# Performance work log

Measured on AMD Instinct MI355X. Metric: run time of the kernel, lower is better.

Reference implementation:

```python
import jax, jax.numpy as jnp
import numpy as np

jax.config.update("jax_enable_x64", True)

VOCAB_R_MAX = 3.0
EPS = 1e-8


def _sanitize(x):
    # torch.nan_to_num(x, nan=0.0, posinf=10000.0, neginf=-10000.0)
    return jnp.nan_to_num(x, nan=0.0, posinf=10000.0, neginf=-10000.0)


def setup_inputs() -> dict:
    key = jax.random.key(0)
    k1, k2 = jax.random.split(key, 2)
    B, L, V, n = 2, 512, 50257, 768
    hidden_states = jax.random.normal(k1, (B, L, n + 1), dtype=jnp.float32)
    # nn.Parameter(torch.randn(V, n) * 0.01) -- tangent vectors
    weight = jax.random.normal(k2, (V, n), dtype=jnp.float32) * 0.01
    # init_temp = 1/sqrt(n_embd)
    logit_scale = jnp.asarray(1.0 / np.sqrt(n), dtype=jnp.float32)
    return {"hidden_states": hidden_states, "weight": weight, "logit_scale": logit_scale}


def _exp_map_zero(v_spatial, max_tangent_norm):
    # Lorentz exp map at origin (curvature -1), tangent vector (0, v_spatial).
    # Norm is clamped to max_tangent_norm (geodesic radius ceiling).
    r = jnp.linalg.norm(v_spatial, axis=-1, keepdims=True)  # [V,1]
    rc = jnp.minimum(r, max_tangent_norm)
    dirv = v_spatial / jnp.maximum(r, EPS)
    return jnp.concatenate([jnp.cosh(rc), jnp.sinh(rc) * dirv], axis=-1)  # [V, n+1]


def _ensure_lorentz(x):
    # Project onto the hyperboloid: x0 = sqrt(1 + ||x_spatial||^2)
    sp = x[..., 1:]
    t = jnp.sqrt(1.0 + jnp.sum(sp * sp, axis=-1, keepdims=True))
    return jnp.concatenate([t, sp], axis=-1)


def reference(hidden_states, weight, logit_scale):
    x = _ensure_lorentz(_sanitize(hidden_states))          # [B,L,n+1]
    w = _sanitize(_exp_map_zero(weight, VOCAB_R_MAX))       # [V,n+1]

    x64 = x.astype(jnp.float64)
    w64 = w.astype(jnp.float64)
    # Minkowski inner product split into time/space einsums (as in source)
    time_inner = jnp.einsum('blt,vt->blv', x64[..., :1], w64[:, :1])
    space_inner = jnp.einsum('bls,vs->blv', x64[..., 1:], w64[:, 1:])
    inner = space_inner - time_inner                        # [B,L,V] fp64

    tau = jnp.clip(logit_scale, 0.01, 2.5).astype(jnp.float64)
    logits = (inner * tau).astype(hidden_states.dtype)
    return _sanitize(logits)
```

## Files before the change

kernel.cpp:

```cpp
#include <hip/hip_runtime.h>
#include <hip/hip_bf16.h>
#include <cstdint>
#include <cstddef>
#include <cstring>

typedef __attribute__((ext_vector_type(4))) float f32x4;
typedef __attribute__((ext_vector_type(8))) short bf16x8;

#define KDIM 768
#define BM 128
#define BN 128
#define BK 64

static __device__ __forceinline__ float sani(float x) {
  if (__builtin_isnan(x)) return 0.0f;
  if (__builtin_isinf(x)) return x > 0.0f ? 1.0e4f : -1.0e4f;
  return x;
}

static __device__ __forceinline__ unsigned short f2bf(float x) {
  unsigned u = __builtin_bit_cast(unsigned, x);
  unsigned r = 0x7FFFu + ((u >> 16) & 1u);
  return (unsigned short)((u + r) >> 16);
}


__global__ __launch_bounds__(256) void prep_x_kernel(
    const float* __restrict__ h, unsigned short* __restrict__ xl,
    float* __restrict__ tx) {
  const int row = blockIdx.x;
  const int t = threadIdx.x;
  const int swz = (row & 7) << 3;
  const float* src = h + (size_t)row * (KDIM + 1) + 1;
  float v0 = sani(src[t]);
  float v1 = sani(src[t + 256]);
  float v2 = sani(src[t + 512]);
  float ss = v0 * v0 + v1 * v1 + v2 * v2;
#pragma unroll
  for (int off = 32; off > 0; off >>= 1) ss += __shfl_down(ss, off);
  __shared__ float red[4];
  if ((t & 63) == 0) red[t >> 6] = ss;
  __syncthreads();
  if (t == 0) {
    float total = red[0] + red[1] + red[2] + red[3];
    tx[row] = sqrtf(1.0f + total);
  }
  unsigned short* dst = xl + (size_t)row * KDIM;
  dst[t ^ swz]         = f2bf(v0);
  dst[(t + 256) ^ swz] = f2bf(v1);
  dst[(t + 512) ^ swz] = f2bf(v2);
}

__global__ __launch_bounds__(256) void prep_w_kernel(
    const float* __restrict__ w, unsigned short* __restrict__ wl,
    float* __restrict__ cw, int V) {
  const int row = blockIdx.x;
  const int t = threadIdx.x;
  const int swz = (row & 7) << 3;
  unsigned short* dst = wl + (size_t)row * KDIM;
  if (row >= V) {
    dst[t] = 0; dst[t + 256] = 0; dst[t + 512] = 0;
    if (t == 0) cw[row] = 0.0f;
    return;
  }
  const float* src = w + (size_t)row * KDIM;
  float v0 = src[t];
  float v1 = src[t + 256];
  float v2 = src[t + 512];
  float ss = v0 * v0 + v1 * v1 + v2 * v2;
#pragma unroll
  for (int off = 32; off > 0; off >>= 1) ss += __shfl_down(ss, off);
  __shared__ float red[4];
  if ((t & 63) == 0) red[t >> 6] = ss;
  __syncthreads();
  float total = red[0] + red[1] + red[2] + red[3];
  float r = sqrtf(total);
  float rc = fminf(r, 3.0f);
  float sc = sinhf(rc) / fmaxf(r, 1e-8f);
  dst[t ^ swz]         = f2bf(sani(v0 * sc));
  dst[(t + 256) ^ swz] = f2bf(sani(v1 * sc));
  dst[(t + 512) ^ swz] = f2bf(sani(v2 * sc));
  if (t == 0) cw[row] = sani(coshf(rc));
}

#define GLD16(gp, sp)                                               \
  __builtin_amdgcn_global_load_lds(                                 \
      (const __attribute__((address_space(1))) void*)(gp),          \
      (__attribute__((address_space(3))) void*)(sp), 16, 0, 0)

__global__ __launch_bounds__(256) void gemm_kernel(
    const unsigned short* __restrict__ xl, const unsigned short* __restrict__ wl,
    const float* __restrict__ tx, const float* __restrict__ cw,
    const float* __restrict__ ls, float* __restrict__ out,
    int V, int Mtiles, int nwg8) {
  __shared__ unsigned short As[BM * BK];
  __shared__ unsigned short Bs[BN * BK];

  const int tid = threadIdx.x;
  const int lane = tid & 63;
  const int wid = tid >> 6;
  const int wr = wid >> 1;
  const int wc = wid & 1;

  const int g = blockIdx.x;
  const int L = (g & 7) * nwg8 + (g >> 3);
  const int bm = L & (Mtiles - 1);
  const int bn = L / Mtiles;

  const int l15 = lane & 15;
  const int lq = lane >> 4;
  const int srow = lane >> 3;
  const int scol = (lane & 7) * 8;
  const int swz = (l15 & 7) << 3;

  f32x4 acc[4][4];
#pragma unroll
  for (int i = 0; i < 4; ++i)
#pragma unroll
    for (int j = 0; j < 4; ++j) acc[i][j] = (f32x4){0.f, 0.f, 0.f, 0.f};

  const size_t a_row0 = (size_t)bm * BM;
  const size_t b_row0 = (size_t)bn * BN;

  for (int kt = 0; kt < KDIM / BK; ++kt) {
    const int kbase = kt * BK;
#pragma unroll
    for (int c = 0; c < 4; ++c) {
      const int chunk = wid * 4 + c;
      const int row = chunk * 8 + srow;
      GLD16(xl + (a_row0 + row) * KDIM + kbase + scol, &As[chunk * 512]);
      GLD16(wl + (b_row0 + row) * KDIM + kbase + scol, &Bs[chunk * 512]);
    }
    asm volatile("s_waitcnt vmcnt(0)" ::: "memory");
    __syncthreads();
#pragma unroll
    for (int kk = 0; kk < 2; ++kk) {
      const int koff = (kk * 32 + lq * 8) ^ swz;
      bf16x8 af[4], bfr[4];
#pragma unroll
      for (int mi = 0; mi < 4; ++mi)
        af[mi] = *(const bf16x8*)&As[(wr * 64 + mi * 16 + l15) * BK + koff];
#pragma unroll
      for (int ni = 0; ni < 4; ++ni)
        bfr[ni] = *(const bf16x8*)&Bs[(wc * 64 + ni * 16 + l15) * BK + koff];
#pragma unroll
      for (int mi = 0; mi < 4; ++mi)
#pragma unroll
        for (int ni = 0; ni < 4; ++ni)
          acc[mi][ni] = __builtin_amdgcn_mfma_f32_16x16x32_bf16(
              bfr[ni], af[mi], acc[mi][ni], 0, 0, 0);
    }
    __syncthreads();
  }

  float tau = ls[0];
  tau = fminf(fmaxf(tau, 0.01f), 2.5f);

#pragma unroll
  for (int mi = 0; mi < 4; ++mi) {
    const int mg = bm * BM + wr * 64 + mi * 16 + l15;
    const float txm = tx[mg];
    float* orow = out + (size_t)mg * V;
#pragma unroll
    for (int ni = 0; ni < 4; ++ni) {
      const int nb = bn * BN + wc * 64 + ni * 16 + lq * 4;
      const f32x4 cw4 = *(const f32x4*)&cw[nb];
      f32x4 v;
#pragma unroll
      for (int j = 0; j < 4; ++j)
        v[j] = (acc[mi][ni][j] - txm * cw4[j]) * tau;
      if (nb + 3 < V) {
        __builtin_memcpy(&orow[nb], &v, 16);
      } else {
#pragma unroll
        for (int j = 0; j < 4; ++j)
          if (nb + j < V) orow[nb + j] = v[j];
      }
    }
  }
}

extern "C" void kernel_launch(void* const* d_in, const int* in_sizes, int n_in,
                              void* d_out, int out_size, void* d_ws, size_t ws_size,
                              hipStream_t stream) {
  const float* h = (const float*)d_in[0];
  const float* w = (const float*)d_in[1];
  const float* ls = (const float*)d_in[2];
  float* out = (float*)d_out;

  const int M = in_sizes[0] / (KDIM + 1);
  const int V = in_sizes[1] / KDIM;
  const int Vpad = (V + BN - 1) & ~(BN - 1);

  char* ws = (char*)d_ws;
  unsigned short* wl = (unsigned short*)ws;
  unsigned short* xl = (unsigned short*)(ws + (size_t)Vpad * KDIM * 2);
  float* cw = (float*)(ws + (size_t)Vpad * KDIM * 2 + (size_t)M * KDIM * 2);
  float* tx = cw + Vpad;

  prep_x_kernel<<<dim3(M), dim3(256), 0, stream>>>(h, xl, tx);
  prep_w_kernel<<<dim3(Vpad), dim3(256), 0, stream>>>(w, wl, cw, V);

  const int Mtiles = M / BM;
  const int nwg = Mtiles * (Vpad / BN);
  gemm_kernel<<<dim3(nwg), dim3(256), 0, stream>>>(
      xl, wl, tx, cw, ls, out, V, Mtiles, nwg / 8);
}
```

Measured before the change: 190.0 us.

## Use 256x256 tiles with 4-stage LDS pipeline and 512-thread workgroups

```diff
diff --git a/kernel.cpp b/kernel.cpp
--- a/kernel.cpp
+++ b/kernel.cpp
@@ -2,15 +2,16 @@
 #include <hip/hip_bf16.h>
 #include <cstdint>
 #include <cstddef>
-#include <cstring>
 
 typedef __attribute__((ext_vector_type(4))) float f32x4;
 typedef __attribute__((ext_vector_type(8))) short bf16x8;
+typedef unsigned short ushort_t;
 
 #define KDIM 768
-#define BM 128
-#define BN 128
-#define BK 64
+#define BM 256
+#define BN 256
+#define BK2 32
+#define NKT 24
 
 static __device__ __forceinline__ float sani(float x) {
   if (__builtin_isnan(x)) return 0.0f;
@@ -26,11 +27,10 @@
 
 
 __global__ __launch_bounds__(256) void prep_x_kernel(
-    const float* __restrict__ h, unsigned short* __restrict__ xl,
+    const float* __restrict__ h, ushort_t* __restrict__ xl,
     float* __restrict__ tx) {
   const int row = blockIdx.x;
   const int t = threadIdx.x;
-  const int swz = (row & 7) << 3;
   const float* src = h + (size_t)row * (KDIM + 1) + 1;
   float v0 = sani(src[t]);
   float v1 = sani(src[t + 256]);
@@ -45,19 +45,18 @@
     float total = red[0] + red[1] + red[2] + red[3];
     tx[row] = sqrtf(1.0f + total);
   }
-  unsigned short* dst = xl + (size_t)row * KDIM;
-  dst[t ^ swz]         = f2bf(v0);
-  dst[(t + 256) ^ swz] = f2bf(v1);
-  dst[(t + 512) ^ swz] = f2bf(v2);
+  ushort_t* dst = xl + (size_t)row * KDIM;
+  dst[t]       = f2bf(v0);
+  dst[t + 256] = f2bf(v1);
+  dst[t + 512] = f2bf(v2);
 }
 
 __global__ __launch_bounds__(256) void prep_w_kernel(
-    const float* __restrict__ w, unsigned short* __restrict__ wl,
+    const float* __restrict__ w, ushort_t* __restrict__ wl,
     float* __restrict__ cw, int V) {
   const int row = blockIdx.x;
   const int t = threadIdx.x;
-  const int swz = (row & 7) << 3;
-  unsigned short* dst = wl + (size_t)row * KDIM;
+  ushort_t* dst = wl + (size_t)row * KDIM;
   if (row >= V) {
     dst[t] = 0; dst[t + 256] = 0; dst[t + 512] = 0;
     if (t == 0) cw[row] = 0.0f;
@@ -77,9 +76,9 @@
   float r = sqrtf(total);
   float rc = fminf(r, 3.0f);
   float sc = sinhf(rc) / fmaxf(r, 1e-8f);
-  dst[t ^ swz]         = f2bf(sani(v0 * sc));
-  dst[(t + 256) ^ swz] = f2bf(sani(v1 * sc));
-  dst[(t + 512) ^ swz] = f2bf(sani(v2 * sc));
+  dst[t]       = f2bf(sani(v0 * sc));
+  dst[t + 256] = f2bf(sani(v1 * sc));
+  dst[t + 512] = f2bf(sani(v2 * sc));
   if (t == 0) cw[row] = sani(coshf(rc));
 }
 
@@ -88,77 +87,97 @@
       (const __attribute__((address_space(1))) void*)(gp),          \
       (__attribute__((address_space(3))) void*)(sp), 16, 0, 0)
 
-__global__ __launch_bounds__(256) void gemm_kernel(
-    const unsigned short* __restrict__ xl, const unsigned short* __restrict__ wl,
+__global__ __launch_bounds__(512, 1) void gemm_kernel(
+    const ushort_t* __restrict__ xl, const ushort_t* __restrict__ wl,
     const float* __restrict__ tx, const float* __restrict__ cw,
     const float* __restrict__ ls, float* __restrict__ out,
-    int V, int Mtiles, int nwg8) {
-  __shared__ unsigned short As[BM * BK];
-  __shared__ unsigned short Bs[BN * BK];
+    int V, int nwg) {
+  __shared__ ushort_t ldsA[4 * 8192];
+  __shared__ ushort_t ldsB[4 * 8192];
 
   const int tid = threadIdx.x;
   const int lane = tid & 63;
   const int wid = tid >> 6;
-  const int wr = wid >> 1;
-  const int wc = wid & 1;
+  const int wr = wid >> 2;
+  const int wc = wid & 3;
 
   const int g = blockIdx.x;
-  const int L = (g & 7) * nwg8 + (g >> 3);
-  const int bm = L & (Mtiles - 1);
-  const int bn = L / Mtiles;
+  const int q = nwg >> 3, rr = nwg & 7;
+  const int xcd = g & 7, lid = g >> 3;
+  const int L = (xcd < rr ? xcd * (q + 1) : rr * (q + 1) + (xcd - rr) * q) + lid;
+  const int bm = L & 3;
+  const int bn = L >> 2;
 
   const int l15 = lane & 15;
   const int lq = lane >> 4;
-  const int srow = lane >> 3;
-  const int scol = (lane & 7) * 8;
-  const int swz = (l15 & 7) << 3;
-
-  f32x4 acc[4][4];
-#pragma unroll
-  for (int i = 0; i < 4; ++i)
-#pragma unroll
-    for (int j = 0; j < 4; ++j) acc[i][j] = (f32x4){0.f, 0.f, 0.f, 0.f};
+  const int g8 = lq * 8;
 
   const size_t a_row0 = (size_t)bm * BM;
   const size_t b_row0 = (size_t)bn * BN;
 
-  for (int kt = 0; kt < KDIM / BK; ++kt) {
-    const int kbase = kt * BK;
-#pragma unroll
-    for (int c = 0; c < 4; ++c) {
-      const int chunk = wid * 4 + c;
-      const int row = chunk * 8 + srow;
-      GLD16(xl + (a_row0 + row) * KDIM + kbase + scol, &As[chunk * 512]);
-      GLD16(wl + (b_row0 + row) * KDIM + kbase + scol, &Bs[chunk * 512]);
-    }
-    asm volatile("s_waitcnt vmcnt(0)" ::: "memory");
-    __syncthreads();
-#pragma unroll
-    for (int kk = 0; kk < 2; ++kk) {
-      const int koff = (kk * 32 + lq * 8) ^ swz;
-      bf16x8 af[4], bfr[4];
-#pragma unroll
-      for (int mi = 0; mi < 4; ++mi)
-        af[mi] = *(const bf16x8*)&As[(wr * 64 + mi * 16 + l15) * BK + koff];
-#pragma unroll
-      for (int ni = 0; ni < 4; ++ni)
-        bfr[ni] = *(const bf16x8*)&Bs[(wc * 64 + ni * 16 + l15) * BK + koff];
-#pragma unroll
-      for (int mi = 0; mi < 4; ++mi)
-#pragma unroll
-        for (int ni = 0; ni < 4; ++ni)
-          acc[mi][ni] = __builtin_amdgcn_mfma_f32_16x16x32_bf16(
-              bfr[ni], af[mi], acc[mi][ni], 0, 0, 0);
-    }
-    __syncthreads();
-  }
+  f32x4 acc[8][4];
+#pragma unroll
+  for (int i = 0; i < 8; ++i)
+#pragma unroll
+    for (int j = 0; j < 4; ++j) acc[i][j] = (f32x4){0.f, 0.f, 0.f, 0.f};
+
+#define STAGE(T)                                                              \
+  {                                                                           \
+    const int slot_ = ((T) & 3) * 8192;                                       \
+    const int kb_ = (T) * BK2 + g8;                                           \
+    GLD16(xl + (a_row0 + wid * 16 + l15) * KDIM + kb_,                        \
+          &ldsA[slot_ + wid * 512]);                                          \
+    GLD16(xl + (a_row0 + (wid + 8) * 16 + l15) * KDIM + kb_,                  \
+          &ldsA[slot_ + (wid + 8) * 512]);                                    \
+    GLD16(wl + (b_row0 + wid * 16 + l15) * KDIM + kb_,                        \
+          &ldsB[slot_ + wid * 512]);                                          \
+    GLD16(wl + (b_row0 + (wid + 8) * 16 + l15) * KDIM + kb_,                  \
+          &ldsB[slot_ + (wid + 8) * 512]);                                    \
+  }
+
+#define COMPUTE(T)                                                            \
+  {                                                                           \
+    const ushort_t* sA_ =                                                     \
+        &ldsA[((T) & 3) * 8192 + wr * 4096 + lq * 128 + l15 * 8];             \
+    const ushort_t* sB_ =                                                     \
+        &ldsB[((T) & 3) * 8192 + wc * 2048 + lq * 128 + l15 * 8];             \
+    bf16x8 bfr[4], afr[8];                                                    \
+    _Pragma("unroll") for (int ni = 0; ni < 4; ++ni)                          \
+        bfr[ni] = *(const bf16x8*)&sB_[ni * 512];                             \
+    _Pragma("unroll") for (int mi = 0; mi < 8; ++mi)                          \
+        afr[mi] = *(const bf16x8*)&sA_[mi * 512];                             \
+    _Pragma("unroll") for (int mi = 0; mi < 8; ++mi)                          \
+      _Pragma("unroll") for (int ni = 0; ni < 4; ++ni)                        \
+          acc[mi][ni] = __builtin_amdgcn_mfma_f32_16x16x32_bf16(              \
+              bfr[ni], afr[mi], acc[mi][ni], 0, 0, 0);                        \
+  }
+
+  STAGE(0);
+  STAGE(1);
+  STAGE(2);
+
+  for (int t = 0; t < NKT - 3; ++t) {
+    asm volatile("s_waitcnt vmcnt(8)\n\ts_barrier" ::: "memory");
+    STAGE(t + 3);
+    __builtin_amdgcn_sched_barrier(0);
+    COMPUTE(t);
+  }
+  asm volatile("s_waitcnt vmcnt(8)\n\ts_barrier" ::: "memory");
+  __builtin_amdgcn_sched_barrier(0);
+  COMPUTE(NKT - 3);
+  asm volatile("s_waitcnt vmcnt(4)\n\ts_barrier" ::: "memory");
+  __builtin_amdgcn_sched_barrier(0);
+  COMPUTE(NKT - 2);
+  asm volatile("s_waitcnt vmcnt(0)\n\ts_barrier" ::: "memory");
+  __builtin_amdgcn_sched_barrier(0);
+  COMPUTE(NKT - 1);
 
   float tau = ls[0];
   tau = fminf(fmaxf(tau, 0.01f), 2.5f);
 
 #pragma unroll
-  for (int mi = 0; mi < 4; ++mi) {
-    const int mg = bm * BM + wr * 64 + mi * 16 + l15;
+  for (int mi = 0; mi < 8; ++mi) {
+    const int mg = bm * BM + wr * 128 + mi * 16 + l15;
     const float txm = tx[mg];
     float* orow = out + (size_t)mg * V;
 #pragma unroll
@@ -178,6 +197,8 @@
       }
     }
   }
+#undef STAGE
+#undef COMPUTE
 }
 
 extern "C" void kernel_launch(void* const* d_in, const int* in_sizes, int n_in,
@@ -193,8 +214,8 @@
   const int Vpad = (V + BN - 1) & ~(BN - 1);
 
   char* ws = (char*)d_ws;
-  unsigned short* wl = (unsigned short*)ws;
-  unsigned short* xl = (unsigned short*)(ws + (size_t)Vpad * KDIM * 2);
+  ushort_t* wl = (ushort_t*)ws;
+  ushort_t* xl = (ushort_t*)(ws + (size_t)Vpad * KDIM * 2);
   float* cw = (float*)(ws + (size_t)Vpad * KDIM * 2 + (size_t)M * KDIM * 2);
   float* tx = cw + Vpad;
 
@@ -203,6 +224,6 @@
 
   const int Mtiles = M / BM;
   const int nwg = Mtiles * (Vpad / BN);
-  gemm_kernel<<<dim3(nwg), dim3(256), 0, stream>>>(
-      xl, wl, tx, cw, ls, out, V, Mtiles, nwg / 8);
-}
+  gemm_kernel<<<dim3(nwg), dim3(512), 0, stream>>>(
+      xl, wl, tx, cw, ls, out, V, nwg);
+}
```

Result: slower. 243.6 us (+28.2%).

## Fuse weight exp-map preprocessing into GEMM with register-staged B prefetch

Applied to the files above, without the earlier changes.

```diff
diff --git a/kernel.cpp b/kernel.cpp
--- a/kernel.cpp
+++ b/kernel.cpp
@@ -2,15 +2,16 @@
 #include <hip/hip_bf16.h>
 #include <cstdint>
 #include <cstddef>
-#include <cstring>
 
 typedef __attribute__((ext_vector_type(4))) float f32x4;
 typedef __attribute__((ext_vector_type(8))) short bf16x8;
+typedef unsigned short ushort_t;
 
 #define KDIM 768
 #define BM 128
 #define BN 128
 #define BK 64
+#define NKT 12
 
 static __device__ __forceinline__ float sani(float x) {
   if (__builtin_isnan(x)) return 0.0f;
@@ -24,9 +25,8 @@
   return (unsigned short)((u + r) >> 16);
 }
 
-
 __global__ __launch_bounds__(256) void prep_x_kernel(
-    const float* __restrict__ h, unsigned short* __restrict__ xl,
+    const float* __restrict__ h, ushort_t* __restrict__ xl,
     float* __restrict__ tx) {
   const int row = blockIdx.x;
   const int t = threadIdx.x;
@@ -45,42 +45,10 @@
     float total = red[0] + red[1] + red[2] + red[3];
     tx[row] = sqrtf(1.0f + total);
   }
-  unsigned short* dst = xl + (size_t)row * KDIM;
+  ushort_t* dst = xl + (size_t)row * KDIM;
   dst[t ^ swz]         = f2bf(v0);
   dst[(t + 256) ^ swz] = f2bf(v1);
   dst[(t + 512) ^ swz] = f2bf(v2);
-}
-
-__global__ __launch_bounds__(256) void prep_w_kernel(
-    const float* __restrict__ w, unsigned short* __restrict__ wl,
-    float* __restrict__ cw, int V) {
-  const int row = blockIdx.x;
-  const int t = threadIdx.x;
-  const int swz = (row & 7) << 3;
-  unsigned short* dst = wl + (size_t)row * KDIM;
-  if (row >= V) {
-    dst[t] = 0; dst[t + 256] = 0; dst[t + 512] = 0;
-    if (t == 0) cw[row] = 0.0f;
-    return;
-  }
-  const float* src = w + (size_t)row * KDIM;
-  float v0 = src[t];
-  float v1 = src[t + 256];
-  float v2 = src[t + 512];
-  float ss = v0 * v0 + v1 * v1 + v2 * v2;
-#pragma unroll
-  for (int off = 32; off > 0; off >>= 1) ss += __shfl_down(ss, off);
-  __shared__ float red[4];
-  if ((t & 63) == 0) red[t >> 6] = ss;
-  __syncthreads();
-  float total = red[0] + red[1] + red[2] + red[3];
-  float r = sqrtf(total);
-  float rc = fminf(r, 3.0f);
-  float sc = sinhf(rc) / fmaxf(r, 1e-8f);
-  dst[t ^ swz]         = f2bf(sani(v0 * sc));
-  dst[(t + 256) ^ swz] = f2bf(sani(v1 * sc));
-  dst[(t + 512) ^ swz] = f2bf(sani(v2 * sc));
-  if (t == 0) cw[row] = sani(coshf(rc));
 }
 
 #define GLD16(gp, sp)                                               \
@@ -89,12 +57,12 @@
       (__attribute__((address_space(3))) void*)(sp), 16, 0, 0)
 
 __global__ __launch_bounds__(256) void gemm_kernel(
-    const unsigned short* __restrict__ xl, const unsigned short* __restrict__ wl,
-    const float* __restrict__ tx, const float* __restrict__ cw,
-    const float* __restrict__ ls, float* __restrict__ out,
-    int V, int Mtiles, int nwg8) {
-  __shared__ unsigned short As[BM * BK];
-  __shared__ unsigned short Bs[BN * BK];
+    const ushort_t* __restrict__ xl, const float* __restrict__ w,
+    const float* __restrict__ tx, const float* __restrict__ ls,
+    float* __restrict__ out, int V, int Mtiles, int nwg8) {
+  __shared__ ushort_t As[BM * BK];
+  __shared__ ushort_t Bs[BN * BK];
+  __shared__ float ssLds[BN];
 
   const int tid = threadIdx.x;
   const int lane = tid & 63;
@@ -113,62 +81,133 @@
   const int scol = (lane & 7) * 8;
   const int swz = (l15 & 7) << 3;
 
+  const int rho = tid >> 4;
+  const int cch = tid & 15;
+
   f32x4 acc[4][4];
 #pragma unroll
   for (int i = 0; i < 4; ++i)
 #pragma unroll
     for (int j = 0; j < 4; ++j) acc[i][j] = (f32x4){0.f, 0.f, 0.f, 0.f};
 
-  const size_t a_row0 = (size_t)bm * BM;
-  const size_t b_row0 = (size_t)bn * BN;
-
-  for (int kt = 0; kt < KDIM / BK; ++kt) {
-    const int kbase = kt * BK;
-#pragma unroll
-    for (int c = 0; c < 4; ++c) {
-      const int chunk = wid * 4 + c;
-      const int row = chunk * 8 + srow;
-      GLD16(xl + (a_row0 + row) * KDIM + kbase + scol, &As[chunk * 512]);
-      GLD16(wl + (b_row0 + row) * KDIM + kbase + scol, &Bs[chunk * 512]);
+  const int a_row0 = bm * BM;
+  const int b_row0 = bn * BN;
+
+  f32x4 breg[8];
+  float ssp[8];
+#pragma unroll
+  for (int i = 0; i < 8; ++i) ssp[i] = 0.0f;
+
+#define LOAD_B(T)                                                             \
+  _Pragma("unroll") for (int i = 0; i < 8; ++i) {                             \
+    int grow = b_row0 + i * 16 + rho;                                         \
+    if (grow >= V) grow = V - 1;                                              \
+    breg[i] = *(const f32x4*)&w[(size_t)grow * KDIM + (T) * BK + cch * 4];    \
+  }
+
+#define WRITE_B()                                                             \
+  _Pragma("unroll") for (int i = 0; i < 8; ++i) {                             \
+    const f32x4 u = breg[i];                                                  \
+    ssp[i] = fmaf(u[0], u[0],                                                 \
+             fmaf(u[1], u[1], fmaf(u[2], u[2], fmaf(u[3], u[3], ssp[i]))));   \
+    float2 flo; flo.x = u[0]; flo.y = u[1];                                   \
+    float2 fhi; fhi.x = u[2]; fhi.y = u[3];                                   \
+    __hip_bfloat162 b0 = __float22bfloat162_rn(flo);                          \
+    __hip_bfloat162 b1 = __float22bfloat162_rn(fhi);                          \
+    uint2 pk;                                                                 \
+    __builtin_memcpy(&pk.x, &b0, 4);                                          \
+    __builtin_memcpy(&pk.y, &b1, 4);                                          \
+    const int row = i * 16 + rho;                                             \
+    *(uint2*)&Bs[row * BK + (((cch >> 1) ^ (row & 7)) << 3) +                 \
+                 ((cch & 1) << 2)] = pk;                                      \
+  }
+
+#define STAGE_A(T)                                                            \
+  _Pragma("unroll") for (int c = 0; c < 4; ++c) {                             \
+    const int chunk = wid * 4 + c;                                            \
+    const int row = chunk * 8 + srow;                                         \
+    GLD16(xl + (size_t)(a_row0 + row) * KDIM + (T) * BK + scol,               \
+          &As[chunk * 512]);                                                  \
+  }
+
+#define COMPUTE()                                                             \
+  _Pragma("unroll") for (int kk = 0; kk < 2; ++kk) {                          \
+    const int koff = (kk * 32 + lq * 8) ^ swz;                                \
+    bf16x8 af[4], bfr[4];                                                     \
+    _Pragma("unroll") for (int mi = 0; mi < 4; ++mi)                          \
+        af[mi] = *(const bf16x8*)&As[(wr * 64 + mi * 16 + l15) * BK + koff];  \
+    _Pragma("unroll") for (int ni = 0; ni < 4; ++ni)                          \
+        bfr[ni] = *(const bf16x8*)&Bs[(wc * 64 + ni * 16 + l15) * BK + koff]; \
+    _Pragma("unroll") for (int mi = 0; mi < 4; ++mi)                          \
+      _Pragma("unroll") for (int ni = 0; ni < 4; ++ni)                        \
+          acc[mi][ni] = __builtin_amdgcn_mfma_f32_16x16x32_bf16(              \
+              bfr[ni], af[mi], acc[mi][ni], 0, 0, 0);                         \
+  }
+
+  LOAD_B(0);
+  for (int t = 0; t < NKT; ++t) {
+    __builtin_amdgcn_s_barrier();
+    __builtin_amdgcn_sched_barrier(0);
+    STAGE_A(t);
+    __builtin_amdgcn_sched_barrier(0);
+    WRITE_B();
+    __builtin_amdgcn_sched_barrier(0);
+    if (t + 1 < NKT) {
+      LOAD_B(t + 1);
+      asm volatile("s_waitcnt vmcnt(8) lgkmcnt(0)" ::: "memory");
+    } else {
+      asm volatile("s_waitcnt vmcnt(0) lgkmcnt(0)" ::: "memory");
     }
-    asm volatile("s_waitcnt vmcnt(0)" ::: "memory");
-    __syncthreads();
-#pragma unroll
-    for (int kk = 0; kk < 2; ++kk) {
-      const int koff = (kk * 32 + lq * 8) ^ swz;
-      bf16x8 af[4], bfr[4];
-#pragma unroll
-      for (int mi = 0; mi < 4; ++mi)
-        af[mi] = *(const bf16x8*)&As[(wr * 64 + mi * 16 + l15) * BK + koff];
-#pragma unroll
-      for (int ni = 0; ni < 4; ++ni)
-        bfr[ni] = *(const bf16x8*)&Bs[(wc * 64 + ni * 16 + l15) * BK + koff];
-#pragma unroll
-      for (int mi = 0; mi < 4; ++mi)
-#pragma unroll
-        for (int ni = 0; ni < 4; ++ni)
-          acc[mi][ni] = __builtin_amdgcn_mfma_f32_16x16x32_bf16(
-              bfr[ni], af[mi], acc[mi][ni], 0, 0, 0);
-    }
-    __syncthreads();
-  }
+    __builtin_amdgcn_s_barrier();
+    __builtin_amdgcn_sched_barrier(0);
+    COMPUTE();
+  }
+
+#pragma unroll
+  for (int i = 0; i < 8; ++i) {
+    float s = ssp[i];
+    s += __shfl_xor(s, 1);
+    s += __shfl_xor(s, 2);
+    s += __shfl_xor(s, 4);
+    s += __shfl_xor(s, 8);
+    ssp[i] = s;
+  }
+  if (cch == 0) {
+#pragma unroll
+    for (int i = 0; i < 8; ++i) ssLds[i * 16 + rho] = ssp[i];
+  }
+  __syncthreads();
 
   float tau = ls[0];
   tau = fminf(fmaxf(tau, 0.01f), 2.5f);
 
+  f32x4 ch4[4], sc4[4];
+#pragma unroll
+  for (int ni = 0; ni < 4; ++ni) {
+    const f32x4 ss4 = *(const f32x4*)&ssLds[wc * 64 + ni * 16 + lq * 4];
+#pragma unroll
+    for (int j = 0; j < 4; ++j) {
+      const float r = sqrtf(ss4[j]);
+      const float rc = fminf(r, 3.0f);
+      const float e = expf(rc);
+      const float ei = 1.0f / e;
+      ch4[ni][j] = 0.5f * (e + ei);
+      sc4[ni][j] = (0.5f * (e - ei)) / fmaxf(r, 1e-8f);
+    }
+  }
+
 #pragma unroll
   for (int mi = 0; mi < 4; ++mi) {
-    const int mg = bm * BM + wr * 64 + mi * 16 + l15;
+    const int mg = a_row0 + wr * 64 + mi * 16 + l15;
     const float txm = tx[mg];
     float* orow = out + (size_t)mg * V;
 #pragma unroll
     for (int ni = 0; ni < 4; ++ni) {
-      const int nb = bn * BN + wc * 64 + ni * 16 + lq * 4;
-      const f32x4 cw4 = *(const f32x4*)&cw[nb];
+      const int nb = b_row0 + wc * 64 + ni * 16 + lq * 4;
       f32x4 v;
 #pragma unroll
       for (int j = 0; j < 4; ++j)
-        v[j] = (acc[mi][ni][j] - txm * cw4[j]) * tau;
+        v[j] = (acc[mi][ni][j] * sc4[ni][j] - txm * ch4[ni][j]) * tau;
       if (nb + 3 < V) {
         __builtin_memcpy(&orow[nb], &v, 16);
       } else {
@@ -178,6 +217,10 @@
       }
     }
   }
+#undef LOAD_B
+#undef WRITE_B
+#undef STAGE_A
+#undef COMPUTE
 }
 
 extern "C" void kernel_launch(void* const* d_in, const int* in_sizes, int n_in,
@@ -193,16 +236,13 @@
   const int Vpad = (V + BN - 1) & ~(BN - 1);
 
   char* ws = (char*)d_ws;
-  unsigned short* wl = (unsigned short*)ws;
-  unsigned short* xl = (unsigned short*)(ws + (size_t)Vpad * KDIM * 2);
-  float* cw = (float*)(ws + (size_t)Vpad * KDIM * 2 + (size_t)M * KDIM * 2);
-  float* tx = cw + Vpad;
+  ushort_t* xl = (ushort_t*)ws;
+  float* tx = (float*)(ws + (size_t)M * KDIM * 2);
 
   prep_x_kernel<<<dim3(M), dim3(256), 0, stream>>>(h, xl, tx);
-  prep_w_kernel<<<dim3(Vpad), dim3(256), 0, stream>>>(w, wl, cw, V);
 
   const int Mtiles = M / BM;
   const int nwg = Mtiles * (Vpad / BN);
   gemm_kernel<<<dim3(nwg), dim3(256), 0, stream>>>(
-      xl, wl, tx, cw, ls, out, V, Mtiles, nwg / 8);
-}
+      xl, w, tx, ls, out, V, Mtiles, nwg / 8);
+}
```

Result: slower. 223.3 us (+17.5%).

## Pre-transpose operands into K-group-major layout and load MFMA fragments from global into registers

Applied to the files above, without the earlier changes.

```diff
diff --git a/kernel.cpp b/kernel.cpp
--- a/kernel.cpp
+++ b/kernel.cpp
@@ -2,15 +2,16 @@
 #include <hip/hip_bf16.h>
 #include <cstdint>
 #include <cstddef>
-#include <cstring>
 
 typedef __attribute__((ext_vector_type(4))) float f32x4;
 typedef __attribute__((ext_vector_type(8))) short bf16x8;
+typedef unsigned short ushort_t;
 
 #define KDIM 768
+#define GQ 96
 #define BM 128
-#define BN 128
-#define BK 64
+#define BN 256
+#define NKT 24
 
 static __device__ __forceinline__ float sani(float x) {
   if (__builtin_isnan(x)) return 0.0f;
@@ -26,11 +27,10 @@
 
 
 __global__ __launch_bounds__(256) void prep_x_kernel(
-    const float* __restrict__ h, unsigned short* __restrict__ xl,
+    const float* __restrict__ h, ushort_t* __restrict__ xt,
     float* __restrict__ tx) {
   const int row = blockIdx.x;
   const int t = threadIdx.x;
-  const int swz = (row & 7) << 3;
   const float* src = h + (size_t)row * (KDIM + 1) + 1;
   float v0 = sani(src[t]);
   float v1 = sani(src[t + 256]);
@@ -45,125 +45,125 @@
     float total = red[0] + red[1] + red[2] + red[3];
     tx[row] = sqrtf(1.0f + total);
   }
-  unsigned short* dst = xl + (size_t)row * KDIM;
-  dst[t ^ swz]         = f2bf(v0);
-  dst[(t + 256) ^ swz] = f2bf(v1);
-  dst[(t + 512) ^ swz] = f2bf(v2);
+  int e;
+  e = t;       xt[((size_t)(e >> 3) * 1024 + row) * 8 + (e & 7)] = f2bf(v0);
+  e = t + 256; xt[((size_t)(e >> 3) * 1024 + row) * 8 + (e & 7)] = f2bf(v1);
+  e = t + 512; xt[((size_t)(e >> 3) * 1024 + row) * 8 + (e & 7)] = f2bf(v2);
 }
 
 __global__ __launch_bounds__(256) void prep_w_kernel(
-    const float* __restrict__ w, unsigned short* __restrict__ wl,
-    float* __restrict__ cw, int V) {
-  const int row = blockIdx.x;
+    const float* __restrict__ w, ushort_t* __restrict__ wt,
+    float* __restrict__ cw, int V, int Vpad) {
+  __shared__ float fs[8 * KDIM];
+  __shared__ float redv[8], scs[8];
   const int t = threadIdx.x;
-  const int swz = (row & 7) << 3;
-  unsigned short* dst = wl + (size_t)row * KDIM;
-  if (row >= V) {
-    dst[t] = 0; dst[t + 256] = 0; dst[t + 512] = 0;
-    if (t == 0) cw[row] = 0.0f;
-    return;
-  }
+  const int r = t >> 5, j = t & 31;
+  const int row = blockIdx.x * 8 + r;
+  const bool valid = row < V;
   const float* src = w + (size_t)row * KDIM;
-  float v0 = src[t];
-  float v1 = src[t + 256];
-  float v2 = src[t + 512];
-  float ss = v0 * v0 + v1 * v1 + v2 * v2;
-#pragma unroll
-  for (int off = 32; off > 0; off >>= 1) ss += __shfl_down(ss, off);
-  __shared__ float red[4];
-  if ((t & 63) == 0) red[t >> 6] = ss;
+  float ss = 0.0f;
+#pragma unroll
+  for (int k = 0; k < 24; ++k) {
+    float v = valid ? src[j + 32 * k] : 0.0f;
+    fs[r * KDIM + j + 32 * k] = v;
+    ss = fmaf(v, v, ss);
+  }
+#pragma unroll
+  for (int m = 16; m > 0; m >>= 1) ss += __shfl_xor(ss, m);
+  if (j == 0) redv[r] = ss;
   __syncthreads();
-  float total = red[0] + red[1] + red[2] + red[3];
-  float r = sqrtf(total);
-  float rc = fminf(r, 3.0f);
-  float sc = sinhf(rc) / fmaxf(r, 1e-8f);
-  dst[t ^ swz]         = f2bf(sani(v0 * sc));
-  dst[(t + 256) ^ swz] = f2bf(sani(v1 * sc));
-  dst[(t + 512) ^ swz] = f2bf(sani(v2 * sc));
-  if (t == 0) cw[row] = sani(coshf(rc));
-}
-
-#define GLD16(gp, sp)                                               \
-  __builtin_amdgcn_global_load_lds(                                 \
-      (const __attribute__((address_space(1))) void*)(gp),          \
-      (__attribute__((address_space(3))) void*)(sp), 16, 0, 0)
-
-__global__ __launch_bounds__(256) void gemm_kernel(
-    const unsigned short* __restrict__ xl, const unsigned short* __restrict__ wl,
+  if (t < 8) {
+    const int rw = blockIdx.x * 8 + t;
+    float rr = sqrtf(redv[t]);
+    float rc = fminf(rr, 3.0f);
+    float e = expf(rc), ei = 1.0f / e;
+    scs[t] = (rw < V) ? 0.5f * (e - ei) / fmaxf(rr, 1e-8f) : 0.0f;
+    cw[rw] = (rw < V) ? sani(0.5f * (e + ei)) : 0.0f;
+  }
+  __syncthreads();
+#pragma unroll
+  for (int p = 0; p < 3; ++p) {
+    const int c = t + 256 * p;
+    const int g = c >> 3, rl = c & 7;
+    const float sc = scs[rl];
+    ushort_t pk[8];
+#pragma unroll
+    for (int e = 0; e < 8; ++e)
+      pk[e] = f2bf(sani(fs[rl * KDIM + g * 8 + e] * sc));
+    *(uint4*)&wt[((size_t)g * Vpad + blockIdx.x * 8 + rl) * 8] =
+        *(const uint4*)pk;
+  }
+}
+
+__global__ __launch_bounds__(256, 2) void gemm_kernel(
+    const ushort_t* __restrict__ xt, const ushort_t* __restrict__ wt,
     const float* __restrict__ tx, const float* __restrict__ cw,
     const float* __restrict__ ls, float* __restrict__ out,
-    int V, int Mtiles, int nwg8) {
-  __shared__ unsigned short As[BM * BK];
-  __shared__ unsigned short Bs[BN * BK];
-
+    int V, int Vpad, int nwg8) {
   const int tid = threadIdx.x;
   const int lane = tid & 63;
-  const int wid = tid >> 6;
-  const int wr = wid >> 1;
-  const int wc = wid & 1;
+  const int wc = tid >> 6;
+  const int l15 = lane & 15;
+  const int lq = lane >> 4;
 
   const int g = blockIdx.x;
   const int L = (g & 7) * nwg8 + (g >> 3);
-  const int bm = L & (Mtiles - 1);
-  const int bn = L / Mtiles;
-
-  const int l15 = lane & 15;
-  const int lq = lane >> 4;
-  const int srow = lane >> 3;
-  const int scol = (lane & 7) * 8;
-  const int swz = (l15 & 7) << 3;
-
-  f32x4 acc[4][4];
-#pragma unroll
-  for (int i = 0; i < 4; ++i)
+  const int bm = L & 7;
+  const int bn = L >> 3;
+
+  const int a_row0 = bm * BM;
+  const int b_row0 = bn * BN + wc * 64;
+
+  const ushort_t* ap = xt + ((size_t)lq * 1024 + a_row0 + l15) * 8;
+  const ushort_t* bp = wt + ((size_t)lq * Vpad + b_row0 + l15) * 8;
+  const size_t astep = (size_t)4 * 1024 * 8;
+  const size_t bstep = (size_t)4 * Vpad * 8;
+
+#define LOADA(T_, D_)                                                         \
+  _Pragma("unroll") for (int mi = 0; mi < 8; ++mi)                            \
+      D_[mi] = *(const bf16x8*)(ap + (size_t)(T_) * astep + mi * 128);
+#define LOADB(T_, D_)                                                         \
+  _Pragma("unroll") for (int ni = 0; ni < 4; ++ni)                            \
+      D_[ni] = *(const bf16x8*)(bp + (size_t)(T_) * bstep + ni * 128);
+#define STEP(AF_, BF_)                                                        \
+  _Pragma("unroll") for (int mi = 0; mi < 8; ++mi)                            \
+    _Pragma("unroll") for (int ni = 0; ni < 4; ++ni)                          \
+        acc[mi][ni] = __builtin_amdgcn_mfma_f32_16x16x32_bf16(                \
+            BF_[ni], AF_[mi], acc[mi][ni], 0, 0, 0);
+
+  f32x4 acc[8][4];
+#pragma unroll
+  for (int i = 0; i < 8; ++i)
 #pragma unroll
     for (int j = 0; j < 4; ++j) acc[i][j] = (f32x4){0.f, 0.f, 0.f, 0.f};
 
-  const size_t a_row0 = (size_t)bm * BM;
-  const size_t b_row0 = (size_t)bn * BN;
-
-  for (int kt = 0; kt < KDIM / BK; ++kt) {
-    const int kbase = kt * BK;
-#pragma unroll
-    for (int c = 0; c < 4; ++c) {
-      const int chunk = wid * 4 + c;
-      const int row = chunk * 8 + srow;
-      GLD16(xl + (a_row0 + row) * KDIM + kbase + scol, &As[chunk * 512]);
-      GLD16(wl + (b_row0 + row) * KDIM + kbase + scol, &Bs[chunk * 512]);
+  bf16x8 afA[8], afB[8], bfA[4], bfB[4];
+  LOADA(0, afA);
+  LOADB(0, bfA);
+#pragma unroll
+  for (int tt = 0; tt < NKT / 2; ++tt) {
+    const int t1 = 2 * tt + 1;
+    LOADA(t1, afB);
+    LOADB(t1, bfB);
+    STEP(afA, bfA);
+    if (t1 + 1 < NKT) {
+      LOADA(t1 + 1, afA);
+      LOADB(t1 + 1, bfA);
     }
-    asm volatile("s_waitcnt vmcnt(0)" ::: "memory");
-    __syncthreads();
-#pragma unroll
-    for (int kk = 0; kk < 2; ++kk) {
-      const int koff = (kk * 32 + lq * 8) ^ swz;
-      bf16x8 af[4], bfr[4];
-#pragma unroll
-      for (int mi = 0; mi < 4; ++mi)
-        af[mi] = *(const bf16x8*)&As[(wr * 64 + mi * 16 + l15) * BK + koff];
-#pragma unroll
-      for (int ni = 0; ni < 4; ++ni)
-        bfr[ni] = *(const bf16x8*)&Bs[(wc * 64 + ni * 16 + l15) * BK + koff];
-#pragma unroll
-      for (int mi = 0; mi < 4; ++mi)
-#pragma unroll
-        for (int ni = 0; ni < 4; ++ni)
-          acc[mi][ni] = __builtin_amdgcn_mfma_f32_16x16x32_bf16(
-              bfr[ni], af[mi], acc[mi][ni], 0, 0, 0);
-    }
-    __syncthreads();
+    STEP(afB, bfB);
   }
 
   float tau = ls[0];
   tau = fminf(fmaxf(tau, 0.01f), 2.5f);
 
 #pragma unroll
-  for (int mi = 0; mi < 4; ++mi) {
-    const int mg = bm * BM + wr * 64 + mi * 16 + l15;
+  for (int mi = 0; mi < 8; ++mi) {
+    const int mg = a_row0 + mi * 16 + l15;
     const float txm = tx[mg];
     float* orow = out + (size_t)mg * V;
 #pragma unroll
     for (int ni = 0; ni < 4; ++ni) {
-      const int nb = bn * BN + wc * 64 + ni * 16 + lq * 4;
+      const int nb = b_row0 + ni * 16 + lq * 4;
       const f32x4 cw4 = *(const f32x4*)&cw[nb];
       f32x4 v;
 #pragma unroll
@@ -178,6 +178,9 @@
       }
     }
   }
+#undef LOADA
+#undef LOADB
+#undef STEP
 }
 
 extern "C" void kernel_launch(void* const* d_in, const int* in_sizes, int n_in,
@@ -193,16 +196,15 @@
   const int Vpad = (V + BN - 1) & ~(BN - 1);
 
   char* ws = (char*)d_ws;
-  unsigned short* wl = (unsigned short*)ws;
-  unsigned short* xl = (unsigned short*)(ws + (size_t)Vpad * KDIM * 2);
-  float* cw = (float*)(ws + (size_t)Vpad * KDIM * 2 + (size_t)M * KDIM * 2);
+  ushort_t* wt = (ushort_t*)ws;
+  ushort_t* xt = (ushort_t*)(ws + (size_t)GQ * Vpad * 8 * 2);
+  float* cw = (float*)(ws + (size_t)GQ * Vpad * 8 * 2 + (size_t)GQ * 1024 * 8 * 2);
   float* tx = cw + Vpad;
 
-  prep_x_kernel<<<dim3(M), dim3(256), 0, stream>>>(h, xl, tx);
-  prep_w_kernel<<<dim3(Vpad), dim3(256), 0, stream>>>(w, wl, cw, V);
-
-  const int Mtiles = M / BM;
-  const int nwg = Mtiles * (Vpad / BN);
+  prep_x_kernel<<<dim3(M), dim3(256), 0, stream>>>(h, xt, tx);
+  prep_w_kernel<<<dim3(Vpad / 8), dim3(256), 0, stream>>>(w, wt, cw, V, Vpad);
+
+  const int nwg = (M / BM) * (Vpad / BN);
   gemm_kernel<<<dim3(nwg), dim3(256), 0, stream>>>(
-      xl, wl, tx, cw, ls, out, V, Mtiles, nwg / 8);
-}
+      xt, wt, tx, cw, ls, out, V, Vpad, nwg / 8);
+}
```

New measurement: 247.7 us. 1.3x slower.
